# Kernel tuning notes

Hardware: AMD Instinct MI355X
Metric: run time of the kernel (lower is better)

The kernel has to match this reference:

```python
import jax, jax.numpy as jnp
import numpy as np
from jax import lax

DT = 0.01
N_STEPS = 2000
BATCH = 8192


def setup_inputs() -> dict:
    key = jax.random.key(0)
    ks = jax.random.split(key, 5)
    # Glorot-ish small init for stability of tanh MLP over many RK4 steps
    return {
        "y0": jax.random.normal(ks[0], (BATCH, 2), dtype=jnp.float32),
        "W1": jax.random.normal(ks[1], (2, 64), dtype=jnp.float32) * 0.5,
        "b1": jnp.zeros((64,), dtype=jnp.float32),
        "W2": jax.random.normal(ks[2], (64, 64), dtype=jnp.float32) * 0.125,
        "b2": jnp.zeros((64,), dtype=jnp.float32),
        "W3": jax.random.normal(ks[3], (64, 2), dtype=jnp.float32) * 0.125,
        "b3": jnp.zeros((2,), dtype=jnp.float32),
    }


def reference(y0, W1, b1, W2, b2, W3, b3):
    def net(y):  # [B,2] -> [B,2]
        h = jnp.tanh(y @ W1 + b1)
        h = jnp.tanh(h @ W2 + b2)
        return h @ W3 + b3

    dt = jnp.float32(DT)

    def rk4_step(y):
        k1 = net(y)
        k2 = net(y + dt * k1 / 2)
        k3 = net(y + dt * k2 / 2)
        k4 = net(y + dt * k3)
        return y + dt / 6 * (k1 + 2 * k2 + 2 * k3 + k4)

    def step_fn(y, _):
        y_next = rk4_step(y)
        return y_next, y_next

    _, ys = lax.scan(step_fn, y0, None, length=N_STEPS)  # [n_steps, B, 2]
    ys = jnp.concatenate([y0[None, ...], ys], axis=0)     # [n_steps+1, B, 2]
    return jnp.transpose(ys, (1, 0, 2))                   # [B, n_steps+1, 2]
```

## Files before the change

### kernel.cpp

```cpp
#include <hip/hip_runtime.h>
#include <stdint.h>

#define N_STEPS 2000
#define DT_F 0.01f

typedef float f32x2 __attribute__((ext_vector_type(2)));

__device__ __forceinline__ float fast_tanh(float x) {
    float e = __builtin_amdgcn_exp2f(x * 2.8853900817779268f);
    float r = __builtin_amdgcn_rcpf(e + 1.0f);
    return fmaf(-2.0f, r, 1.0f);
}

__device__ __forceinline__ float rl(float v, int lane) {
    return __builtin_bit_cast(float, __builtin_amdgcn_readlane(__builtin_bit_cast(int, v), lane));
}

template <int CTRL>
__device__ __forceinline__ float dpp_add(float v) {
    return v + __builtin_bit_cast(float, __builtin_amdgcn_update_dpp(
                   0, __builtin_bit_cast(int, v), CTRL, 0xf, 0xf, true));
}

__device__ __forceinline__ float wave_sum_s(float v) {
    v = dpp_add<0x111>(v);
    v = dpp_add<0x112>(v);
    v = dpp_add<0x114>(v);
    v = dpp_add<0x118>(v);
    v = dpp_add<0x142>(v);
    v = dpp_add<0x143>(v);
    return rl(v, 63);
}

__global__ __attribute__((amdgpu_flat_work_group_size(256, 256),
                          amdgpu_waves_per_eu(2, 2)))
void node_rk4_kernel(
    const float* __restrict__ y0_in,
    const float* __restrict__ W1, const float* __restrict__ B1,
    const float* __restrict__ W2, const float* __restrict__ B2,
    const float* __restrict__ W3, const float* __restrict__ B3,
    float* __restrict__ out, int batch)
{
    __shared__ __align__(16) float sW2T[64 * 64];
    __shared__ __align__(16) float hl_all[4][64];

    const int tid  = threadIdx.x;
    const int lane = tid & 63;
    const int wib  = tid >> 6;
    const int b    = blockIdx.x * 4 + wib;

    for (int idx = tid; idx < 64 * 64; idx += 256) {
        sW2T[(idx & 63) * 64 + (idx >> 6)] = W2[idx];
    }
    __syncthreads();

    if (b >= batch) return;

    const int j = lane;
    const float w1_0 = W1[j], w1_1 = W1[64 + j];
    const float b1v  = B1[j], b2v = B2[j];
    const float w3_0 = W3[2 * j], w3_1 = W3[2 * j + 1];
    const float b3l0 = (lane == 0) ? B3[0] : 0.0f;
    const float b3l1 = (lane == 0) ? B3[1] : 0.0f;

    f32x2 w2p[32];
    {
        volatile const float* col = sW2T + (j << 6);
        #pragma unroll
        for (int i = 0; i < 32; ++i) {
            w2p[i].x = col[2 * i];
            w2p[i].y = col[2 * i + 1];
        }
    }

    float y0 = y0_in[2 * b + 0];
    float y1 = y0_in[2 * b + 1];

    float* outb = out + (size_t)b * (2 * (N_STEPS + 1));
    if (lane == 0) {
        reinterpret_cast<float2*>(outb)[0] = make_float2(y0, y1);
    }

    float chdt = 0.5f * DT_F, cdt = DT_F, cdt6 = DT_F / 6.0f;
    asm("" : "+v"(chdt), "+v"(cdt), "+v"(cdt6));

    float* hl = hl_all[wib];
    const f32x2* hp2 = (const f32x2*)hl;

    auto net = [&](float yi0, float yi1, float& o0, float& o1) {
        float pre = fmaf(yi0, w1_0, fmaf(yi1, w1_1, b1v));
        float h1  = fast_tanh(pre);
        hl[lane] = h1;
        __builtin_amdgcn_wave_barrier();

        f32x2 acc0 = (f32x2){b2v, 0.0f};
        f32x2 acc1 = (f32x2){0.0f, 0.0f};
        f32x2 acc2 = (f32x2){0.0f, 0.0f};
        f32x2 acc3 = (f32x2){0.0f, 0.0f};
        #pragma unroll
        for (int i = 0; i < 32; i += 4) {
            acc0 = __builtin_elementwise_fma(hp2[i + 0], w2p[i + 0], acc0);
            acc1 = __builtin_elementwise_fma(hp2[i + 1], w2p[i + 1], acc1);
            acc2 = __builtin_elementwise_fma(hp2[i + 2], w2p[i + 2], acc2);
            acc3 = __builtin_elementwise_fma(hp2[i + 3], w2p[i + 3], acc3);
        }
        __builtin_amdgcn_wave_barrier();

        f32x2 s = (acc0 + acc1) + (acc2 + acc3);
        float h2 = fast_tanh(s.x + s.y);
        float p0 = fmaf(h2, w3_0, b3l0);
        float p1 = fmaf(h2, w3_1, b3l1);
        o0 = wave_sum_s(p0);
        o1 = wave_sum_s(p1);
    };

    for (int t = 1; t <= N_STEPS; ++t) {
        float k10, k11, k20, k21, k30, k31, k40, k41;
        net(y0, y1, k10, k11);
        net(fmaf(chdt, k10, y0), fmaf(chdt, k11, y1), k20, k21);
        net(fmaf(chdt, k20, y0), fmaf(chdt, k21, y1), k30, k31);
        net(fmaf(cdt,  k30, y0), fmaf(cdt,  k31, y1), k40, k41);
        float s0 = (k10 + k40) + 2.0f * (k20 + k30);
        float s1 = (k11 + k41) + 2.0f * (k21 + k31);
        y0 = fmaf(cdt6, s0, y0);
        y1 = fmaf(cdt6, s1, y1);
        if (lane == 0) {
            reinterpret_cast<float2*>(outb)[t] = make_float2(y0, y1);
        }
    }
}

extern "C" void kernel_launch(void* const* d_in, const int* in_sizes, int n_in,
                              void* d_out, int out_size, void* d_ws, size_t ws_size,
                              hipStream_t stream) {
    const float* y0 = (const float*)d_in[0];
    const float* W1 = (const float*)d_in[1];
    const float* B1 = (const float*)d_in[2];
    const float* W2 = (const float*)d_in[3];
    const float* B2 = (const float*)d_in[4];
    const float* W3 = (const float*)d_in[5];
    const float* B3 = (const float*)d_in[6];
    float* out = (float*)d_out;

    const int batch = in_sizes[0] / 2;
    const int blocks = (batch + 3) / 4;

    node_rk4_kernel<<<blocks, 256, 0, stream>>>(y0, W1, B1, W2, B2, W3, B3, out, batch);
}
```

Before: 12.05 ms.

## Process two batch rows per wave with bpermute-based split reductions

Each wave now integrates two independent trajectories, interleaving their MLP evaluations to expose instruction-level parallelism and halving the grid size. The DPP+readlane wave reduction is replaced with a ds_bpermute butterfly where each half-wave reduces a different output component, and the W2 transpose in LDS is padded to 66 columns to avoid bank conflicts. Hidden-vector reads from LDS are widened to 4-float loads. The costs are higher register pressure, fewer waves in the grid (4096 instead of 8192), and bpermute going through the LDS path. No bB < batch check exists, so an odd batch would go out of bounds.

```diff
diff --git a/kernel.cpp b/kernel.cpp
--- a/kernel.cpp
+++ b/kernel.cpp
@@ -5,6 +5,7 @@
 #define DT_F 0.01f
 
 typedef float f32x2 __attribute__((ext_vector_type(2)));
+typedef float f32x4 __attribute__((ext_vector_type(4)));
 
 __device__ __forceinline__ float fast_tanh(float x) {
     float e = __builtin_amdgcn_exp2f(x * 2.8853900817779268f);
@@ -12,24 +13,28 @@
     return fmaf(-2.0f, r, 1.0f);
 }
 
-__device__ __forceinline__ float rl(float v, int lane) {
-    return __builtin_bit_cast(float, __builtin_amdgcn_readlane(__builtin_bit_cast(int, v), lane));
+__device__ __forceinline__ float bperm(float v, int addr) {
+    return __builtin_bit_cast(float, __builtin_amdgcn_ds_bpermute(
+               addr, __builtin_bit_cast(int, v)));
 }
 
-template <int CTRL>
-__device__ __forceinline__ float dpp_add(float v) {
-    return v + __builtin_bit_cast(float, __builtin_amdgcn_update_dpp(
-                   0, __builtin_bit_cast(int, v), CTRL, 0xf, 0xf, true));
-}
+__device__ __forceinline__ f32x2 lo2(f32x4 v) { return __builtin_shufflevector(v, v, 0, 1); }
+__device__ __forceinline__ f32x2 hi2(f32x4 v) { return __builtin_shufflevector(v, v, 2, 3); }
 
-__device__ __forceinline__ float wave_sum_s(float v) {
-    v = dpp_add<0x111>(v);
-    v = dpp_add<0x112>(v);
-    v = dpp_add<0x114>(v);
-    v = dpp_add<0x118>(v);
-    v = dpp_add<0x142>(v);
-    v = dpp_add<0x143>(v);
-    return rl(v, 63);
+__device__ __forceinline__ void kreduce(float p0, float p1, bool half0,
+                                        int a1, int a2, int a4, int a8,
+                                        int a16, int a32,
+                                        float& kq, float& kr) {
+    float f0 = p0 + bperm(p0, a32);
+    float f1 = p1 + bperm(p1, a32);
+    float q  = half0 ? f0 : f1;
+    q += bperm(q, a1);
+    q += bperm(q, a2);
+    q += bperm(q, a4);
+    q += bperm(q, a8);
+    q += bperm(q, a16);
+    kq = q;
+    kr = bperm(q, a32);
 }
 
 __global__ __attribute__((amdgpu_flat_work_group_size(256, 256),
@@ -41,31 +46,36 @@
     const float* __restrict__ W3, const float* __restrict__ B3,
     float* __restrict__ out, int batch)
 {
-    __shared__ __align__(16) float sW2T[64 * 64];
-    __shared__ __align__(16) float hl_all[4][64];
+    __shared__ __align__(16) float sW2T[64 * 66];
+    __shared__ __align__(16) float hl_all[4][2][64];
 
     const int tid  = threadIdx.x;
     const int lane = tid & 63;
     const int wib  = tid >> 6;
-    const int b    = blockIdx.x * 4 + wib;
+    const int w    = blockIdx.x * 4 + wib;
+    const int bA   = 2 * w;
+    const int bB   = 2 * w + 1;
 
     for (int idx = tid; idx < 64 * 64; idx += 256) {
-        sW2T[(idx & 63) * 64 + (idx >> 6)] = W2[idx];
+        sW2T[(idx & 63) * 66 + (idx >> 6)] = W2[idx];
     }
     __syncthreads();
 
-    if (b >= batch) return;
+    if (bA >= batch) return;
 
-    const int j = lane;
-    const float w1_0 = W1[j], w1_1 = W1[64 + j];
-    const float b1v  = B1[j], b2v = B2[j];
+    const int  j     = lane;
+    const bool half0 = (lane < 32);
+
+    const float wqv = half0 ? W1[j] : W1[64 + j];
+    const float wrv = half0 ? W1[64 + j] : W1[j];
+    const float b1v = B1[j], b2v = B2[j];
     const float w3_0 = W3[2 * j], w3_1 = W3[2 * j + 1];
     const float b3l0 = (lane == 0) ? B3[0] : 0.0f;
     const float b3l1 = (lane == 0) ? B3[1] : 0.0f;
 
     f32x2 w2p[32];
     {
-        volatile const float* col = sW2T + (j << 6);
+        volatile const float* col = sW2T + j * 66;
         #pragma unroll
         for (int i = 0; i < 32; ++i) {
             w2p[i].x = col[2 * i];
@@ -73,59 +83,89 @@
         }
     }
 
-    float y0 = y0_in[2 * b + 0];
-    float y1 = y0_in[2 * b + 1];
+    const int a1  = ((lane ^ 1)  << 2);
+    const int a2  = ((lane ^ 2)  << 2);
+    const int a4  = ((lane ^ 4)  << 2);
+    const int a8  = ((lane ^ 8)  << 2);
+    const int a16 = ((lane ^ 16) << 2);
+    const int a32 = ((lane ^ 32) << 2);
 
-    float* outb = out + (size_t)b * (2 * (N_STEPS + 1));
+    float yA0 = y0_in[2 * bA], yA1 = y0_in[2 * bA + 1];
+    float yB0 = y0_in[2 * bB], yB1 = y0_in[2 * bB + 1];
+    float yAq = half0 ? yA0 : yA1, yAr = half0 ? yA1 : yA0;
+    float yBq = half0 ? yB0 : yB1, yBr = half0 ? yB1 : yB0;
+
+    float* outA = out + (size_t)bA * (2 * (N_STEPS + 1));
+    float* outB = out + (size_t)bB * (2 * (N_STEPS + 1));
     if (lane == 0) {
-        reinterpret_cast<float2*>(outb)[0] = make_float2(y0, y1);
+        reinterpret_cast<float2*>(outA)[0] = make_float2(yAq, yAr);
+        reinterpret_cast<float2*>(outB)[0] = make_float2(yBq, yBr);
     }
 
-    float chdt = 0.5f * DT_F, cdt = DT_F, cdt6 = DT_F / 6.0f;
-    asm("" : "+v"(chdt), "+v"(cdt), "+v"(cdt6));
+    float* hlA = hl_all[wib][0];
+    float* hlB = hl_all[wib][1];
+    const f32x4* hpA4 = (const f32x4*)hlA;
+    const f32x4* hpB4 = (const f32x4*)hlB;
 
-    float* hl = hl_all[wib];
-    const f32x2* hp2 = (const f32x2*)hl;
+    const float chdt = 0.5f * DT_F, cdt = DT_F, cdt6 = DT_F / 6.0f;
 
-    auto net = [&](float yi0, float yi1, float& o0, float& o1) {
-        float pre = fmaf(yi0, w1_0, fmaf(yi1, w1_1, b1v));
-        float h1  = fast_tanh(pre);
-        hl[lane] = h1;
+    auto net2 = [&](float iAq, float iAr, float iBq, float iBr,
+                    float& kAq, float& kAr, float& kBq, float& kBr) {
+        float hA = fast_tanh(fmaf(wqv, iAq, fmaf(wrv, iAr, b1v)));
+        float hB = fast_tanh(fmaf(wqv, iBq, fmaf(wrv, iBr, b1v)));
+        hlA[lane] = hA;
+        hlB[lane] = hB;
         __builtin_amdgcn_wave_barrier();
 
-        f32x2 acc0 = (f32x2){b2v, 0.0f};
-        f32x2 acc1 = (f32x2){0.0f, 0.0f};
-        f32x2 acc2 = (f32x2){0.0f, 0.0f};
-        f32x2 acc3 = (f32x2){0.0f, 0.0f};
+        f32x2 aA0 = (f32x2){b2v, 0.0f}, aA1 = (f32x2){0.0f, 0.0f};
+        f32x2 aA2 = (f32x2){0.0f, 0.0f}, aA3 = (f32x2){0.0f, 0.0f};
+        f32x2 aB0 = (f32x2){b2v, 0.0f}, aB1 = (f32x2){0.0f, 0.0f};
+        f32x2 aB2 = (f32x2){0.0f, 0.0f}, aB3 = (f32x2){0.0f, 0.0f};
         #pragma unroll
-        for (int i = 0; i < 32; i += 4) {
-            acc0 = __builtin_elementwise_fma(hp2[i + 0], w2p[i + 0], acc0);
-            acc1 = __builtin_elementwise_fma(hp2[i + 1], w2p[i + 1], acc1);
-            acc2 = __builtin_elementwise_fma(hp2[i + 2], w2p[i + 2], acc2);
-            acc3 = __builtin_elementwise_fma(hp2[i + 3], w2p[i + 3], acc3);
+        for (int c = 0; c < 16; c += 2) {
+            f32x4 hA0 = hpA4[c], hA1 = hpA4[c + 1];
+            f32x4 hB0 = hpB4[c], hB1 = hpB4[c + 1];
+            aA0 = __builtin_elementwise_fma(lo2(hA0), w2p[2 * c + 0], aA0);
+            aA1 = __builtin_elementwise_fma(hi2(hA0), w2p[2 * c + 1], aA1);
+            aA2 = __builtin_elementwise_fma(lo2(hA1), w2p[2 * c + 2], aA2);
+            aA3 = __builtin_elementwise_fma(hi2(hA1), w2p[2 * c + 3], aA3);
+            aB0 = __builtin_elementwise_fma(lo2(hB0), w2p[2 * c + 0], aB0);
+            aB1 = __builtin_elementwise_fma(hi2(hB0), w2p[2 * c + 1], aB1);
+            aB2 = __builtin_elementwise_fma(lo2(hB1), w2p[2 * c + 2], aB2);
+            aB3 = __builtin_elementwise_fma(hi2(hB1), w2p[2 * c + 3], aB3);
         }
         __builtin_amdgcn_wave_barrier();
 
-        f32x2 s = (acc0 + acc1) + (acc2 + acc3);
-        float h2 = fast_tanh(s.x + s.y);
-        float p0 = fmaf(h2, w3_0, b3l0);
-        float p1 = fmaf(h2, w3_1, b3l1);
-        o0 = wave_sum_s(p0);
-        o1 = wave_sum_s(p1);
+        f32x2 sA = (aA0 + aA1) + (aA2 + aA3);
+        f32x2 sB = (aB0 + aB1) + (aB2 + aB3);
+        float h2A = fast_tanh(sA.x + sA.y);
+        float h2B = fast_tanh(sB.x + sB.y);
+        float pA0 = fmaf(h2A, w3_0, b3l0), pA1 = fmaf(h2A, w3_1, b3l1);
+        float pB0 = fmaf(h2B, w3_0, b3l0), pB1 = fmaf(h2B, w3_1, b3l1);
+        kreduce(pA0, pA1, half0, a1, a2, a4, a8, a16, a32, kAq, kAr);
+        kreduce(pB0, pB1, half0, a1, a2, a4, a8, a16, a32, kBq, kBr);
     };
 
     for (int t = 1; t <= N_STEPS; ++t) {
-        float k10, k11, k20, k21, k30, k31, k40, k41;
-        net(y0, y1, k10, k11);
-        net(fmaf(chdt, k10, y0), fmaf(chdt, k11, y1), k20, k21);
-        net(fmaf(chdt, k20, y0), fmaf(chdt, k21, y1), k30, k31);
-        net(fmaf(cdt,  k30, y0), fmaf(cdt,  k31, y1), k40, k41);
-        float s0 = (k10 + k40) + 2.0f * (k20 + k30);
-        float s1 = (k11 + k41) + 2.0f * (k21 + k31);
-        y0 = fmaf(cdt6, s0, y0);
-        y1 = fmaf(cdt6, s1, y1);
+        float k1Aq, k1Ar, k1Bq, k1Br, k2Aq, k2Ar, k2Bq, k2Br;
+        float k3Aq, k3Ar, k3Bq, k3Br, k4Aq, k4Ar, k4Bq, k4Br;
+        net2(yAq, yAr, yBq, yBr, k1Aq, k1Ar, k1Bq, k1Br);
+        net2(fmaf(chdt, k1Aq, yAq), fmaf(chdt, k1Ar, yAr),
+             fmaf(chdt, k1Bq, yBq), fmaf(chdt, k1Br, yBr),
+             k2Aq, k2Ar, k2Bq, k2Br);
+        net2(fmaf(chdt, k2Aq, yAq), fmaf(chdt, k2Ar, yAr),
+             fmaf(chdt, k2Bq, yBq), fmaf(chdt, k2Br, yBr),
+             k3Aq, k3Ar, k3Bq, k3Br);
+        net2(fmaf(cdt, k3Aq, yAq), fmaf(cdt, k3Ar, yAr),
+             fmaf(cdt, k3Bq, yBq), fmaf(cdt, k3Br, yBr),
+             k4Aq, k4Ar, k4Bq, k4Br);
+        yAq = fmaf(cdt6, (k1Aq + k4Aq) + 2.0f * (k2Aq + k3Aq), yAq);
+        yAr = fmaf(cdt6, (k1Ar + k4Ar) + 2.0f * (k2Ar + k3Ar), yAr);
+        yBq = fmaf(cdt6, (k1Bq + k4Bq) + 2.0f * (k2Bq + k3Bq), yBq);
+        yBr = fmaf(cdt6, (k1Br + k4Br) + 2.0f * (k2Br + k3Br), yBr);
         if (lane == 0) {
-            reinterpret_cast<float2*>(outb)[t] = make_float2(y0, y1);
+            reinterpret_cast<float2*>(outA)[t] = make_float2(yAq, yAr);
+            reinterpret_cast<float2*>(outB)[t] = make_float2(yBq, yBr);
         }
     }
 }
@@ -143,7 +183,7 @@
     float* out = (float*)d_out;
 
     const int batch = in_sizes[0] / 2;
-    const int blocks = (batch + 3) / 4;
+    const int blocks = (batch + 7) / 8;
 
     node_rk4_kernel<<<blocks, 256, 0, stream>>>(y0, W1, B1, W2, B2, W3, B3, out, batch);
 }
```

After: 14.25 ms. 1.18x slower.
